# Kernel optimization log

Measured on AMD Instinct MI355X. Metric: run time of the kernel, lower is better.

The kernel has to match this reference:

```python
import jax, jax.numpy as jnp
import numpy as np

B, N, F = 4096, 128, 3
EPS = 1e-5


def _bn(x, g, b):
    # BatchNorm1d(element_num) on [B, N, C]: channels are dim 1 (the N elements);
    # training-mode stats over dims (0, 2), biased variance (torch default).
    m = x.mean(axis=(0, 2), keepdims=True)
    v = ((x - m) ** 2).mean(axis=(0, 2), keepdims=True)
    return (x - m) / jnp.sqrt(v + EPS) * g[None, :, None] + b[None, :, None]


def _rel(x, W, bvec, psi, phi, wr):
    # f'_i = wr/N * sum_{j != i} (psi*phi * <x_i, x_j>) * relu(unary(x_j))
    n = x.shape[1]
    U = jax.nn.relu(jnp.einsum('bnd,ed->bne', x, W) + bvec)       # [B,N,D]
    S = (psi * phi) * jnp.einsum('bnd,bmd->bnm', x, x)            # [B,N,N]
    S = S * (1.0 - jnp.eye(n, dtype=x.dtype))                     # exclude j == i
    return wr * jnp.einsum('bnm,bmd->bnd', S, U) / n


def setup_inputs() -> dict:
    key = jax.random.key(0)
    ks = iter(jax.random.split(key, 64))
    d1, d2 = 2 * F, 4 * F  # 6, 12

    def w(shape, s=0.1):
        return (jax.random.normal(next(ks), shape, dtype=jnp.float32) * s)

    def scalar():
        return jax.random.uniform(next(ks), (), dtype=jnp.float32)

    inp = {
        'x': jax.random.normal(next(ks), (B, N, F), dtype=jnp.float32),
        'fc1_w': w((d1, F)), 'fc1_b': w((d1,)),
        'bn1_g': jnp.ones((N,), jnp.float32), 'bn1_b': jnp.zeros((N,), jnp.float32),
        'fc2_w': w((d2, d1)), 'fc2_b': w((d2,)),
        'bn2_g': jnp.ones((N,), jnp.float32), 'bn2_b': jnp.zeros((N,), jnp.float32),
        'fc3_w': w((d2, d2)), 'fc3_b': w((d2,)),
        'u1_w': w((d2, d2)), 'u1_b': w((d2,)), 'ps1': scalar(), 'ph1': scalar(), 'wr1': scalar(),
        'u2_w': w((d2, d2)), 'u2_b': w((d2,)), 'ps2': scalar(), 'ph2': scalar(), 'wr2': scalar(),
        'u3_w': w((d2, d2)), 'u3_b': w((d2,)), 'ps3': scalar(), 'ph3': scalar(), 'wr3': scalar(),
        'u4_w': w((d2, d2)), 'u4_b': w((d2,)), 'ps4': scalar(), 'ph4': scalar(), 'wr4': scalar(),
        'fc4_w': w((d1, d2)), 'fc4_b': w((d1,)),
        'bn4_g': jnp.ones((N,), jnp.float32), 'bn4_b': jnp.zeros((N,), jnp.float32),
        'fc5_w': w((F, d1)), 'fc5_b': w((F,)),
        'fc6_w': w((1, F)), 'fc6_b': w((1,)),
        'fc7_w': w((F - 1, F)), 'fc7_b': w((F - 1,)),
        'fc8_w': w((1, F)), 'fc8_b': w((1,)),
    }
    return inp


def reference(x, fc1_w, fc1_b, bn1_g, bn1_b, fc2_w, fc2_b, bn2_g, bn2_b,
              fc3_w, fc3_b,
              u1_w, u1_b, ps1, ph1, wr1,
              u2_w, u2_b, ps2, ph2, wr2,
              u3_w, u3_b, ps3, ph3, wr3,
              u4_w, u4_b, ps4, ph4, wr4,
              fc4_w, fc4_b, bn4_g, bn4_b,
              fc5_w, fc5_b, fc6_w, fc6_b, fc7_w, fc7_b, fc8_w, fc8_b):
    h = jax.nn.relu(_bn(jnp.einsum('bnf,ef->bne', x, fc1_w) + fc1_b, bn1_g, bn1_b))
    h = jax.nn.relu(_bn(jnp.einsum('bnf,ef->bne', h, fc2_w) + fc2_b, bn2_g, bn2_b))
    h = jax.nn.sigmoid(jnp.einsum('bnf,ef->bne', h, fc3_w) + fc3_b)
    h = _rel(h, u1_w, u1_b, ps1, ph1, wr1)
    h = _rel(h, u2_w, u2_b, ps2, ph2, wr2)
    h = _rel(h, u3_w, u3_b, ps3, ph3, wr3)
    h = _rel(h, u4_w, u4_b, ps4, ph4, wr4)
    h = jax.nn.relu(_bn(jnp.einsum('bnf,ef->bne', h, fc4_w) + fc4_b, bn4_g, bn4_b))
    h = jax.nn.relu(jnp.einsum('bnf,ef->bne', h, fc5_w) + fc5_b)
    cls = jnp.einsum('bnf,ef->bne', h, fc6_w) + fc6_b          # [B,N,1]
    geo = jnp.einsum('bnf,ef->bne', h, fc7_w) + fc7_b          # [B,N,F-1]
    res = jnp.concatenate([cls, geo], axis=2)                   # [B,N,F]
    pres = res.max(axis=1)                                      # MaxPool1d over all N -> [B,F]
    pred = jax.nn.sigmoid(pres @ fc8_w.T + fc8_b)               # [B,1]
    return pred
```

## Files before the change

### kernel.cpp

```cpp
#include <hip/hip_runtime.h>
#include <hip/hip_fp16.h>

#define BB 4096
#define NN 128
#define EPS 1e-5f

#define ST_FLOATS 2560
#define A4_OFF ST_FLOATS

static __device__ __forceinline__ float sigmoidf_(float z){
  return 1.f/(1.f+__expf(-z));
}

__global__ __launch_bounds__(256) void k1(const float* __restrict__ x, const float* __restrict__ w1,
                   const float* __restrict__ b1, float* __restrict__ st){
  __shared__ float bl[512];
  const int t = threadIdx.x;
  const int tid = blockIdx.x*256 + t;
  const int n = tid & 127;
  float W[18], Bv[6];
  #pragma unroll
  for (int i=0;i<18;i++) W[i]=w1[i];
  #pragma unroll
  for (int i=0;i<6;i++) Bv[i]=b1[i];
  float s=0.f, sq=0.f;
  #pragma unroll
  for (int kk=0;kk<16;kk++){
    const int r = tid + kk*32768;
    const float* xr = x + (size_t)r*3;
    float x0=xr[0], x1=xr[1], x2=xr[2];
    #pragma unroll
    for (int e=0;e<6;e++){
      float a = fmaf(x0,W[e*3+0], fmaf(x1,W[e*3+1], fmaf(x2,W[e*3+2], Bv[e])));
      s+=a; sq=fmaf(a,a,sq);
    }
  }
  bl[t]=s; bl[256+t]=sq;
  __syncthreads();
  if (t<128){
    atomicAdd(&st[t], bl[t]+bl[t+128]);
  } else {
    const int tt=t-128;
    atomicAdd(&st[128+tt], bl[256+tt]+bl[256+tt+128]);
  }
}

__global__ __launch_bounds__(256) void k2(const float* __restrict__ x,
                   const float* __restrict__ w1, const float* __restrict__ b1,
                   const float* __restrict__ g1, const float* __restrict__ bb1,
                   const float* __restrict__ w2, const float* __restrict__ b2,
                   float* __restrict__ st){
  __shared__ float bl[512];
  const int t = threadIdx.x;
  const int tid = blockIdx.x*256 + t;
  const int n = tid & 127;
  const float mean = st[n]*(1.f/(BB*6));
  const float var  = st[128+n]*(1.f/(BB*6)) - mean*mean;
  const float sc = g1[n]*rsqrtf(var+EPS), sh = bb1[n]-mean*sc;
  float W1[18], B1v[6], W2[72], B2v[12];
  #pragma unroll
  for (int i=0;i<18;i++) W1[i]=w1[i];
  #pragma unroll
  for (int i=0;i<6;i++) B1v[i]=b1[i];
  #pragma unroll
  for (int i=0;i<72;i++) W2[i]=w2[i];
  #pragma unroll
  for (int i=0;i<12;i++) B2v[i]=b2[i];
  float s=0.f, sq=0.f;
  #pragma unroll
  for (int kk=0;kk<16;kk++){
    const int r = tid + kk*32768;
    const float* xr = x + (size_t)r*3;
    float x0=xr[0], x1=xr[1], x2=xr[2];
    float h[6];
    #pragma unroll
    for (int e=0;e<6;e++){
      float a = fmaf(x0,W1[e*3+0], fmaf(x1,W1[e*3+1], fmaf(x2,W1[e*3+2], B1v[e])));
      h[e]=fmaxf(fmaf(a,sc,sh),0.f);
    }
    #pragma unroll
    for (int d=0;d<12;d++){
      float z=B2v[d];
      #pragma unroll
      for (int e=0;e<6;e++) z=fmaf(h[e],W2[d*6+e],z);
      s+=z; sq=fmaf(z,z,sq);
    }
  }
  bl[t]=s; bl[256+t]=sq;
  __syncthreads();
  if (t<128){
    atomicAdd(&st[256+t], bl[t]+bl[t+128]);
  } else {
    const int tt=t-128;
    atomicAdd(&st[384+tt], bl[256+tt]+bl[256+tt+128]);
  }
}

__global__ __launch_bounds__(256,4) void k3(
  const float* __restrict__ x,
  const float* __restrict__ w1, const float* __restrict__ b1,
  const float* __restrict__ g1, const float* __restrict__ bb1,
  const float* __restrict__ w2, const float* __restrict__ b2,
  const float* __restrict__ g2, const float* __restrict__ bb2,
  const float* __restrict__ w3, const float* __restrict__ b3,
  const float* __restrict__ u1w, const float* __restrict__ u1b,
  const float* __restrict__ ps1, const float* __restrict__ ph1, const float* __restrict__ wr1,
  const float* __restrict__ u2w, const float* __restrict__ u2b,
  const float* __restrict__ ps2, const float* __restrict__ ph2, const float* __restrict__ wr2,
  const float* __restrict__ u3w, const float* __restrict__ u3b,
  const float* __restrict__ ps3, const float* __restrict__ ph3, const float* __restrict__ wr3,
  const float* __restrict__ u4w, const float* __restrict__ u4b,
  const float* __restrict__ ps4, const float* __restrict__ ph4, const float* __restrict__ wr4,
  const float* __restrict__ w4, const float* __restrict__ b4,
  float* __restrict__ a4, float* __restrict__ st)
{
  __shared__ float lds[4][2304];
  const int wave = threadIdx.x >> 6;
  const int lane = threadIdx.x & 63;
  const int b = blockIdx.x*4 + wave;
  float* Us = &lds[wave][0];
  __half* Xs = (__half*)&lds[wave][1536];
  const int r0 = lane*2, r1 = r0+1;

  const float inv1 = 1.f/(BB*6);
  const float m10 = st[r0]*inv1, v10 = st[128+r0]*inv1 - m10*m10;
  const float sA0 = g1[r0]*rsqrtf(v10+EPS), hA0 = bb1[r0]-m10*sA0;
  const float m11 = st[r1]*inv1, v11 = st[128+r1]*inv1 - m11*m11;
  const float sA1 = g1[r1]*rsqrtf(v11+EPS), hA1 = bb1[r1]-m11*sA1;
  const float inv2 = 1.f/(BB*12);
  const float m20 = st[256+r0]*inv2, v20 = st[384+r0]*inv2 - m20*m20;
  const float sB0 = g2[r0]*rsqrtf(v20+EPS), hB0 = bb2[r0]-m20*sB0;
  const float m21 = st[256+r1]*inv2, v21 = st[384+r1]*inv2 - m21*m21;
  const float sB1 = g2[r1]*rsqrtf(v21+EPS), hB1 = bb2[r1]-m21*sB1;

  const float2* xr = (const float2*)(x + ((size_t)b*128 + r0)*3);
  float2 q0v=xr[0], q1v=xr[1], q2v=xr[2], q3v=xr[3], q4v=xr[4], q5v=xr[5];
  const float xa0=q0v.x, xa1=q0v.y, xa2=q1v.x;
  const float xb0=q1v.y, xb1=q2v.x, xb2=q2v.y;
  (void)q3v; (void)q4v; (void)q5v;

  float h0[12], h1[12];
  {
    float g6a[6], g6b[6];
    #pragma unroll
    for (int e=0;e<6;e++){
      float a0 = fmaf(xa0,w1[e*3+0], fmaf(xa1,w1[e*3+1], fmaf(xa2,w1[e*3+2], b1[e])));
      float a1v= fmaf(xb0,w1[e*3+0], fmaf(xb1,w1[e*3+1], fmaf(xb2,w1[e*3+2], b1[e])));
      g6a[e]=fmaxf(fmaf(a0,sA0,hA0),0.f);
      g6b[e]=fmaxf(fmaf(a1v,sA1,hA1),0.f);
    }
    #pragma unroll
    for (int d=0;d<12;d++){
      float z0=b2[d], z1=b2[d];
      #pragma unroll
      for (int e=0;e<6;e++){ z0=fmaf(g6a[e],w2[d*6+e],z0); z1=fmaf(g6b[e],w2[d*6+e],z1); }
      h0[d]=fmaxf(fmaf(z0,sB0,hB0),0.f);
      h1[d]=fmaxf(fmaf(z1,sB1,hB1),0.f);
    }
  }

  float X0[12], X1[12];
  #pragma unroll
  for (int d=0; d<12; d++){
    float z0=b3[d], z1=b3[d];
    #pragma unroll
    for (int e=0;e<12;e++){ z0=fmaf(h0[e],w3[d*12+e],z0); z1=fmaf(h1[e],w3[d*12+e],z1); }
    X0[d]=sigmoidf_(z0); X1[d]=sigmoidf_(z1);
  }

  const float* UW[4]  = {u1w,u2w,u3w,u4w};
  const float* UBv[4] = {u1b,u2b,u3b,u4b};
  const float cf[4] = {
    wr1[0]*ps1[0]*ph1[0]*(1.f/128.f),
    wr2[0]*ps2[0]*ph2[0]*(1.f/128.f),
    wr3[0]*ps3[0]*ph3[0]*(1.f/128.f),
    wr4[0]*ps4[0]*ph4[0]*(1.f/128.f)
  };

  const int g = lane>>4;
  int kc = lane & 15; if (kc>11) kc=11;

  #pragma unroll
  for (int l=0;l<4;l++){
    const float* uw = UW[l];
    const float* ub = UBv[l];
    float U0[12], U1[12];
    #pragma unroll
    for (int d=0;d<12;d++){
      float z0=ub[d], z1=ub[d];
      #pragma unroll
      for (int e=0;e<12;e++){ z0=fmaf(X0[e],uw[d*12+e],z0); z1=fmaf(X1[e],uw[d*12+e],z1); }
      U0[d]=fmaxf(z0,0.f); U1[d]=fmaxf(z1,0.f);
    }
    float q0=0.f, q1=0.f;
    #pragma unroll
    for (int e=0;e<12;e++){ q0=fmaf(X0[e],X0[e],q0); q1=fmaf(X1[e],X1[e],q1); }

    float4* uwr = (float4*)(Us + r0*12);
    uwr[0]=make_float4(U0[0],U0[1],U0[2],U0[3]);
    uwr[1]=make_float4(U0[4],U0[5],U0[6],U0[7]);
    uwr[2]=make_float4(U0[8],U0[9],U0[10],U0[11]);
    uwr[3]=make_float4(U1[0],U1[1],U1[2],U1[3]);
    uwr[4]=make_float4(U1[4],U1[5],U1[6],U1[7]);
    uwr[5]=make_float4(U1[8],U1[9],U1[10],U1[11]);
    __half2 hp[12];
    #pragma unroll
    for (int i=0;i<6;i++) hp[i]   = __floats2half2_rn(X0[2*i],X0[2*i+1]);
    #pragma unroll
    for (int i=0;i<6;i++) hp[6+i] = __floats2half2_rn(X1[2*i],X1[2*i+1]);
    {
      const uint4* hpv = (const uint4*)hp;
      uint4* xw = (uint4*)(Xs + r0*12);
      xw[0]=hpv[0]; xw[1]=hpv[1]; xw[2]=hpv[2];
    }

    float mp[12];
    #pragma unroll
    for (int d=0;d<12;d++) mp[d]=0.f;
    #pragma unroll
    for (int i=0;i<32;i++){
      const int n = (g<<5) + ((i+g)&31);
      const float xv = __half2float(Xs[n*12 + kc]);
      const float4* up = (const float4*)(Us + n*12);
      float4 u0=up[0], u1=up[1], u2=up[2];
      mp[0]=fmaf(xv,u0.x,mp[0]); mp[1]=fmaf(xv,u0.y,mp[1]); mp[2]=fmaf(xv,u0.z,mp[2]); mp[3]=fmaf(xv,u0.w,mp[3]);
      mp[4]=fmaf(xv,u1.x,mp[4]); mp[5]=fmaf(xv,u1.y,mp[5]); mp[6]=fmaf(xv,u1.z,mp[6]); mp[7]=fmaf(xv,u1.w,mp[7]);
      mp[8]=fmaf(xv,u2.x,mp[8]); mp[9]=fmaf(xv,u2.y,mp[9]); mp[10]=fmaf(xv,u2.z,mp[10]); mp[11]=fmaf(xv,u2.w,mp[11]);
    }
    #pragma unroll
    for (int d=0;d<12;d++) mp[d] += __shfl_xor(mp[d], 16, 64);
    #pragma unroll
    for (int d=0;d<12;d++) mp[d] += __shfl_xor(mp[d], 32, 64);

    float Y0[12], Y1[12];
    #pragma unroll
    for (int d=0;d<12;d++){ Y0[d]=0.f; Y1[d]=0.f; }
    #pragma unroll
    for (int k=0;k<12;k++){
      const float xa = X0[k], xb = X1[k];
      #pragma unroll
      for (int d=0;d<12;d++){
        const float m = __int_as_float(__builtin_amdgcn_readlane(__float_as_int(mp[d]), k));
        Y0[d]=fmaf(xa,m,Y0[d]); Y1[d]=fmaf(xb,m,Y1[d]);
      }
    }
    const float coef = cf[l];
    #pragma unroll
    for (int d=0;d<12;d++){
      X0[d] = coef*(Y0[d] - q0*U0[d]);
      X1[d] = coef*(Y1[d] - q1*U1[d]);
    }
  }

  float z0[6], z1[6];
  float s0=0.f,sq0=0.f,s1=0.f,sq1=0.f;
  #pragma unroll
  for (int e=0;e<6;e++){
    float a0=b4[e], a1v=b4[e];
    #pragma unroll
    for (int d=0;d<12;d++){ a0=fmaf(X0[d],w4[e*12+d],a0); a1v=fmaf(X1[d],w4[e*12+d],a1v); }
    z0[e]=a0; z1[e]=a1v;
    s0+=a0; sq0=fmaf(a0,a0,sq0); s1+=a1v; sq1=fmaf(a1v,a1v,sq1);
  }
  float4* aw = (float4*)(a4 + ((size_t)b*128 + r0)*6);
  aw[0]=make_float4(z0[0],z0[1],z0[2],z0[3]);
  aw[1]=make_float4(z0[4],z0[5],z1[0],z1[1]);
  aw[2]=make_float4(z1[2],z1[3],z1[4],z1[5]);

  lds[wave][r0]=s0; lds[wave][r1]=s1;
  lds[wave][128+r0]=sq0; lds[wave][128+r1]=sq1;
  __syncthreads();
  const int t = threadIdx.x;
  const int c = (blockIdx.x & 7)*256;
  if (t < 128){
    float tot = lds[0][t]+lds[1][t]+lds[2][t]+lds[3][t];
    atomicAdd(&st[512 + c + t], tot);
  } else {
    const int tt = t-128;
    float tot = lds[0][128+tt]+lds[1][128+tt]+lds[2][128+tt]+lds[3][128+tt];
    atomicAdd(&st[512 + c + 128 + tt], tot);
  }
}

__global__ __launch_bounds__(256) void k4(
  const float* __restrict__ a4, const float* __restrict__ g4, const float* __restrict__ bb4,
  const float* __restrict__ w5, const float* __restrict__ b5,
  const float* __restrict__ w6, const float* __restrict__ b6,
  const float* __restrict__ w7, const float* __restrict__ b7,
  const float* __restrict__ w8, const float* __restrict__ b8,
  const float* __restrict__ st, float* __restrict__ out)
{
  const int wave = threadIdx.x>>6, lane = threadIdx.x&63;
  const int b = blockIdx.x*4 + wave;
  const int r0 = lane*2, r1 = r0+1;
  float ss0=0.f, qq0=0.f, ss1=0.f, qq1=0.f;
  #pragma unroll
  for (int cc=0;cc<8;cc++){
    ss0 += st[512+cc*256+r0];     qq0 += st[512+cc*256+128+r0];
    ss1 += st[512+cc*256+r1];     qq1 += st[512+cc*256+128+r1];
  }
  const float inv = 1.f/(BB*6);
  const float mean0 = ss0*inv, var0 = qq0*inv - mean0*mean0;
  const float sc0 = g4[r0]*rsqrtf(var0+EPS), sh0 = bb4[r0]-mean0*sc0;
  const float mean1 = ss1*inv, var1 = qq1*inv - mean1*mean1;
  const float sc1 = g4[r1]*rsqrtf(var1+EPS), sh1 = bb4[r1]-mean1*sc1;

  const float4* ar = (const float4*)(a4 + ((size_t)b*128 + r0)*6);
  float4 p0=ar[0], p1=ar[1], p2=ar[2];
  float h0[6] = {p0.x,p0.y,p0.z,p0.w,p1.x,p1.y};
  float h1[6] = {p1.z,p1.w,p2.x,p2.y,p2.z,p2.w};
  #pragma unroll
  for (int e=0;e<6;e++){
    h0[e]=fmaxf(fmaf(h0[e],sc0,sh0),0.f);
    h1[e]=fmaxf(fmaf(h1[e],sc1,sh1),0.f);
  }
  float m[3];
  {
    float h5a[3], h5b[3];
    #pragma unroll
    for (int f=0;f<3;f++){
      float za=b5[f], zb=b5[f];
      #pragma unroll
      for (int e=0;e<6;e++){ za=fmaf(h0[e],w5[f*6+e],za); zb=fmaf(h1[e],w5[f*6+e],zb); }
      h5a[f]=fmaxf(za,0.f); h5b[f]=fmaxf(zb,0.f);
    }
    float ca=b6[0], cb=b6[0];
    float g0a=b7[0], g0b=b7[0], g1a=b7[1], g1b=b7[1];
    #pragma unroll
    for (int f=0;f<3;f++){
      ca=fmaf(h5a[f],w6[f],ca);   cb=fmaf(h5b[f],w6[f],cb);
      g0a=fmaf(h5a[f],w7[f],g0a); g0b=fmaf(h5b[f],w7[f],g0b);
      g1a=fmaf(h5a[f],w7[3+f],g1a); g1b=fmaf(h5b[f],w7[3+f],g1b);
    }
    m[0]=fmaxf(ca,cb); m[1]=fmaxf(g0a,g0b); m[2]=fmaxf(g1a,g1b);
  }
  #pragma unroll
  for (int off=32; off>0; off>>=1){
    m[0]=fmaxf(m[0], __shfl_xor(m[0],off,64));
    m[1]=fmaxf(m[1], __shfl_xor(m[1],off,64));
    m[2]=fmaxf(m[2], __shfl_xor(m[2],off,64));
  }
  if (lane==0){
    float z = b8[0] + m[0]*w8[0] + m[1]*w8[1] + m[2]*w8[2];
    out[b]=sigmoidf_(z);
  }
}

extern "C" void kernel_launch(void* const* d_in, const int* in_sizes, int n_in,
                              void* d_out, int out_size, void* d_ws, size_t ws_size,
                              hipStream_t stream){
  const float* x   = (const float*)d_in[0];
  const float* f1w = (const float*)d_in[1];
  const float* f1b = (const float*)d_in[2];
  const float* g1  = (const float*)d_in[3];
  const float* bb1 = (const float*)d_in[4];
  const float* f2w = (const float*)d_in[5];
  const float* f2b = (const float*)d_in[6];
  const float* g2  = (const float*)d_in[7];
  const float* bb2 = (const float*)d_in[8];
  const float* f3w = (const float*)d_in[9];
  const float* f3b = (const float*)d_in[10];
  const float* u1w = (const float*)d_in[11];
  const float* u1b = (const float*)d_in[12];
  const float* ps1 = (const float*)d_in[13];
  const float* ph1 = (const float*)d_in[14];
  const float* wr1 = (const float*)d_in[15];
  const float* u2w = (const float*)d_in[16];
  const float* u2b = (const float*)d_in[17];
  const float* ps2 = (const float*)d_in[18];
  const float* ph2 = (const float*)d_in[19];
  const float* wr2 = (const float*)d_in[20];
  const float* u3w = (const float*)d_in[21];
  const float* u3b = (const float*)d_in[22];
  const float* ps3 = (const float*)d_in[23];
  const float* ph3 = (const float*)d_in[24];
  const float* wr3 = (const float*)d_in[25];
  const float* u4w = (const float*)d_in[26];
  const float* u4b = (const float*)d_in[27];
  const float* ps4 = (const float*)d_in[28];
  const float* ph4 = (const float*)d_in[29];
  const float* wr4 = (const float*)d_in[30];
  const float* f4w = (const float*)d_in[31];
  const float* f4b = (const float*)d_in[32];
  const float* g4  = (const float*)d_in[33];
  const float* bb4 = (const float*)d_in[34];
  const float* f5w = (const float*)d_in[35];
  const float* f5b = (const float*)d_in[36];
  const float* f6w = (const float*)d_in[37];
  const float* f6b = (const float*)d_in[38];
  const float* f7w = (const float*)d_in[39];
  const float* f7b = (const float*)d_in[40];
  const float* f8w = (const float*)d_in[41];
  const float* f8b = (const float*)d_in[42];

  float* wsf = (float*)d_ws;
  float* st  = wsf;
  float* a4  = wsf + A4_OFF;
  float* out = (float*)d_out;

  hipMemsetAsync(st, 0, ST_FLOATS*sizeof(float), stream);
  k1<<<dim3(128), dim3(256), 0, stream>>>(x, f1w, f1b, st);
  k2<<<dim3(128), dim3(256), 0, stream>>>(x, f1w, f1b, g1, bb1, f2w, f2b, st);
  k3<<<dim3(1024), dim3(256), 0, stream>>>(x, f1w, f1b, g1, bb1, f2w, f2b, g2, bb2,
      f3w, f3b,
      u1w,u1b,ps1,ph1,wr1, u2w,u2b,ps2,ph2,wr2,
      u3w,u3b,ps3,ph3,wr3, u4w,u4b,ps4,ph4,wr4,
      f4w, f4b, a4, st);
  k4<<<dim3(1024), dim3(256), 0, stream>>>(a4, g4, bb4, f5w, f5b,
      f6w, f6b, f7w, f7b, f8w, f8b, st, out);
}
```

Measured before the change: 220.4 us.

## Widen BN stat kernels to 1024 blocks with shadowed atomic accumulators

The BN1/BN2 statistics kernels now launch 1024 blocks with 2 rows per thread instead of 128 blocks looping 16 times, which spreads the work over more CUs. To limit contention on the atomics, each block adds into one of 8 shadow copies of the stat arrays, and consumers sum those copies. The main kernel drops its occupancy hint of 4 from launch bounds, scopes h0/h1 more tightly, and folds the -q*U term into the accumulator initialisation. It also adds a __syncthreads before reusing LDS for the partial stats. Consumers now do 8x more stat reads, and register allocation may shift without the occupancy hint.

```diff
diff --git a/kernel.cpp b/kernel.cpp
--- a/kernel.cpp
+++ b/kernel.cpp
@@ -5,8 +5,11 @@
 #define NN 128
 #define EPS 1e-5f
 
-#define ST_FLOATS 2560
-#define A4_OFF ST_FLOATS
+#define S1 0
+#define S2 2048
+#define S4 4096
+#define ST_FLOATS 6144
+#define A4_OFF 6144
 
 static __device__ __forceinline__ float sigmoidf_(float z){
   return 1.f/(1.f+__expf(-z));
@@ -17,7 +20,6 @@
   __shared__ float bl[512];
   const int t = threadIdx.x;
   const int tid = blockIdx.x*256 + t;
-  const int n = tid & 127;
   float W[18], Bv[6];
   #pragma unroll
   for (int i=0;i<18;i++) W[i]=w1[i];
@@ -25,8 +27,8 @@
   for (int i=0;i<6;i++) Bv[i]=b1[i];
   float s=0.f, sq=0.f;
   #pragma unroll
-  for (int kk=0;kk<16;kk++){
-    const int r = tid + kk*32768;
+  for (int kk=0;kk<2;kk++){
+    const int r = tid + kk*262144;
     const float* xr = x + (size_t)r*3;
     float x0=xr[0], x1=xr[1], x2=xr[2];
     #pragma unroll
@@ -37,12 +39,9 @@
   }
   bl[t]=s; bl[256+t]=sq;
   __syncthreads();
-  if (t<128){
-    atomicAdd(&st[t], bl[t]+bl[t+128]);
-  } else {
-    const int tt=t-128;
-    atomicAdd(&st[128+tt], bl[256+tt]+bl[256+tt+128]);
-  }
+  const int shadow = (blockIdx.x & 7)*256;
+  if (t<128) atomicAdd(&st[S1+shadow+t], bl[t]+bl[t+128]);
+  else       atomicAdd(&st[S1+shadow+t], bl[t+128]+bl[t+256]);
 }
 
 __global__ __launch_bounds__(256) void k2(const float* __restrict__ x,
@@ -53,9 +52,12 @@
   __shared__ float bl[512];
   const int t = threadIdx.x;
   const int tid = blockIdx.x*256 + t;
-  const int n = tid & 127;
-  const float mean = st[n]*(1.f/(BB*6));
-  const float var  = st[128+n]*(1.f/(BB*6)) - mean*mean;
+  const int n = t & 127;
+  float ss=0.f, qs=0.f;
+  #pragma unroll
+  for (int c=0;c<8;c++){ ss+=st[S1+c*256+n]; qs+=st[S1+c*256+128+n]; }
+  const float mean = ss*(1.f/(BB*6));
+  const float var  = qs*(1.f/(BB*6)) - mean*mean;
   const float sc = g1[n]*rsqrtf(var+EPS), sh = bb1[n]-mean*sc;
   float W1[18], B1v[6], W2[72], B2v[12];
   #pragma unroll
@@ -68,8 +70,8 @@
   for (int i=0;i<12;i++) B2v[i]=b2[i];
   float s=0.f, sq=0.f;
   #pragma unroll
-  for (int kk=0;kk<16;kk++){
-    const int r = tid + kk*32768;
+  for (int kk=0;kk<2;kk++){
+    const int r = tid + kk*262144;
     const float* xr = x + (size_t)r*3;
     float x0=xr[0], x1=xr[1], x2=xr[2];
     float h[6];
@@ -88,15 +90,12 @@
   }
   bl[t]=s; bl[256+t]=sq;
   __syncthreads();
-  if (t<128){
-    atomicAdd(&st[256+t], bl[t]+bl[t+128]);
-  } else {
-    const int tt=t-128;
-    atomicAdd(&st[384+tt], bl[256+tt]+bl[256+tt+128]);
-  }
-}
-
-__global__ __launch_bounds__(256,4) void k3(
+  const int shadow = (blockIdx.x & 7)*256;
+  if (t<128) atomicAdd(&st[S2+shadow+t], bl[t]+bl[t+128]);
+  else       atomicAdd(&st[S2+shadow+t], bl[t+128]+bl[t+256]);
+}
+
+__global__ __launch_bounds__(256) void k3(
   const float* __restrict__ x,
   const float* __restrict__ w1, const float* __restrict__ b1,
   const float* __restrict__ g1, const float* __restrict__ bb1,
@@ -122,24 +121,30 @@
   __half* Xs = (__half*)&lds[wave][1536];
   const int r0 = lane*2, r1 = r0+1;
 
-  const float inv1 = 1.f/(BB*6);
-  const float m10 = st[r0]*inv1, v10 = st[128+r0]*inv1 - m10*m10;
-  const float sA0 = g1[r0]*rsqrtf(v10+EPS), hA0 = bb1[r0]-m10*sA0;
-  const float m11 = st[r1]*inv1, v11 = st[128+r1]*inv1 - m11*m11;
-  const float sA1 = g1[r1]*rsqrtf(v11+EPS), hA1 = bb1[r1]-m11*sA1;
-  const float inv2 = 1.f/(BB*12);
-  const float m20 = st[256+r0]*inv2, v20 = st[384+r0]*inv2 - m20*m20;
-  const float sB0 = g2[r0]*rsqrtf(v20+EPS), hB0 = bb2[r0]-m20*sB0;
-  const float m21 = st[256+r1]*inv2, v21 = st[384+r1]*inv2 - m21*m21;
-  const float sB1 = g2[r1]*rsqrtf(v21+EPS), hB1 = bb2[r1]-m21*sB1;
+  float s1a=0,q1a=0,s1b=0,q1b=0,s2a=0,q2a=0,s2b=0,q2b=0;
+  #pragma unroll
+  for (int c=0;c<8;c++){
+    s1a+=st[S1+c*256+r0]; q1a+=st[S1+c*256+128+r0];
+    s1b+=st[S1+c*256+r1]; q1b+=st[S1+c*256+128+r1];
+    s2a+=st[S2+c*256+r0]; q2a+=st[S2+c*256+128+r0];
+    s2b+=st[S2+c*256+r1]; q2b+=st[S2+c*256+128+r1];
+  }
+  const float inv1 = 1.f/(BB*6), inv2 = 1.f/(BB*12);
+  float m = s1a*inv1, v = q1a*inv1 - m*m;
+  const float sA0 = g1[r0]*rsqrtf(v+EPS), hA0 = bb1[r0]-m*sA0;
+  m = s1b*inv1; v = q1b*inv1 - m*m;
+  const float sA1 = g1[r1]*rsqrtf(v+EPS), hA1 = bb1[r1]-m*sA1;
+  m = s2a*inv2; v = q2a*inv2 - m*m;
+  const float sB0 = g2[r0]*rsqrtf(v+EPS), hB0 = bb2[r0]-m*sB0;
+  m = s2b*inv2; v = q2b*inv2 - m*m;
+  const float sB1 = g2[r1]*rsqrtf(v+EPS), hB1 = bb2[r1]-m*sB1;
 
   const float2* xr = (const float2*)(x + ((size_t)b*128 + r0)*3);
-  float2 q0v=xr[0], q1v=xr[1], q2v=xr[2], q3v=xr[3], q4v=xr[4], q5v=xr[5];
-  const float xa0=q0v.x, xa1=q0v.y, xa2=q1v.x;
-  const float xb0=q1v.y, xb1=q2v.x, xb2=q2v.y;
-  (void)q3v; (void)q4v; (void)q5v;
-
-  float h0[12], h1[12];
+  float2 c0=xr[0], c1=xr[1], c2=xr[2];
+  const float xa0=c0.x, xa1=c0.y, xa2=c1.x;
+  const float xb0=c1.y, xb1=c2.x, xb2=c2.y;
+
+  float X0[12], X1[12];
   {
     float g6a[6], g6b[6];
     #pragma unroll
@@ -149,6 +154,7 @@
       g6a[e]=fmaxf(fmaf(a0,sA0,hA0),0.f);
       g6b[e]=fmaxf(fmaf(a1v,sA1,hA1),0.f);
     }
+    float h0[12], h1[12];
     #pragma unroll
     for (int d=0;d<12;d++){
       float z0=b2[d], z1=b2[d];
@@ -157,15 +163,13 @@
       h0[d]=fmaxf(fmaf(z0,sB0,hB0),0.f);
       h1[d]=fmaxf(fmaf(z1,sB1,hB1),0.f);
     }
-  }
-
-  float X0[12], X1[12];
-  #pragma unroll
-  for (int d=0; d<12; d++){
-    float z0=b3[d], z1=b3[d];
-    #pragma unroll
-    for (int e=0;e<12;e++){ z0=fmaf(h0[e],w3[d*12+e],z0); z1=fmaf(h1[e],w3[d*12+e],z1); }
-    X0[d]=sigmoidf_(z0); X1[d]=sigmoidf_(z1);
+    #pragma unroll
+    for (int d=0; d<12; d++){
+      float z0=b3[d], z1=b3[d];
+      #pragma unroll
+      for (int e=0;e<12;e++){ z0=fmaf(h0[e],w3[d*12+e],z0); z1=fmaf(h1[e],w3[d*12+e],z1); }
+      X0[d]=sigmoidf_(z0); X1[d]=sigmoidf_(z1);
+    }
   }
 
   const float* UW[4]  = {u1w,u2w,u3w,u4w};
@@ -184,34 +188,38 @@
   for (int l=0;l<4;l++){
     const float* uw = UW[l];
     const float* ub = UBv[l];
-    float U0[12], U1[12];
-    #pragma unroll
-    for (int d=0;d<12;d++){
-      float z0=ub[d], z1=ub[d];
-      #pragma unroll
-      for (int e=0;e<12;e++){ z0=fmaf(X0[e],uw[d*12+e],z0); z1=fmaf(X1[e],uw[d*12+e],z1); }
-      U0[d]=fmaxf(z0,0.f); U1[d]=fmaxf(z1,0.f);
-    }
-    float q0=0.f, q1=0.f;
-    #pragma unroll
-    for (int e=0;e<12;e++){ q0=fmaf(X0[e],X0[e],q0); q1=fmaf(X1[e],X1[e],q1); }
-
-    float4* uwr = (float4*)(Us + r0*12);
-    uwr[0]=make_float4(U0[0],U0[1],U0[2],U0[3]);
-    uwr[1]=make_float4(U0[4],U0[5],U0[6],U0[7]);
-    uwr[2]=make_float4(U0[8],U0[9],U0[10],U0[11]);
-    uwr[3]=make_float4(U1[0],U1[1],U1[2],U1[3]);
-    uwr[4]=make_float4(U1[4],U1[5],U1[6],U1[7]);
-    uwr[5]=make_float4(U1[8],U1[9],U1[10],U1[11]);
-    __half2 hp[12];
-    #pragma unroll
-    for (int i=0;i<6;i++) hp[i]   = __floats2half2_rn(X0[2*i],X0[2*i+1]);
-    #pragma unroll
-    for (int i=0;i<6;i++) hp[6+i] = __floats2half2_rn(X1[2*i],X1[2*i+1]);
+    float Y0[12], Y1[12];
     {
-      const uint4* hpv = (const uint4*)hp;
-      uint4* xw = (uint4*)(Xs + r0*12);
-      xw[0]=hpv[0]; xw[1]=hpv[1]; xw[2]=hpv[2];
+      float U0[12], U1[12];
+      #pragma unroll
+      for (int d=0;d<12;d++){
+        float z0=ub[d], z1=ub[d];
+        #pragma unroll
+        for (int e=0;e<12;e++){ z0=fmaf(X0[e],uw[d*12+e],z0); z1=fmaf(X1[e],uw[d*12+e],z1); }
+        U0[d]=fmaxf(z0,0.f); U1[d]=fmaxf(z1,0.f);
+      }
+      float q0=0.f, q1=0.f;
+      #pragma unroll
+      for (int e=0;e<12;e++){ q0=fmaf(X0[e],X0[e],q0); q1=fmaf(X1[e],X1[e],q1); }
+      float4* uwr = (float4*)(Us + r0*12);
+      uwr[0]=make_float4(U0[0],U0[1],U0[2],U0[3]);
+      uwr[1]=make_float4(U0[4],U0[5],U0[6],U0[7]);
+      uwr[2]=make_float4(U0[8],U0[9],U0[10],U0[11]);
+      uwr[3]=make_float4(U1[0],U1[1],U1[2],U1[3]);
+      uwr[4]=make_float4(U1[4],U1[5],U1[6],U1[7]);
+      uwr[5]=make_float4(U1[8],U1[9],U1[10],U1[11]);
+      __half2 hp[12];
+      #pragma unroll
+      for (int i=0;i<6;i++) hp[i]   = __floats2half2_rn(X0[2*i],X0[2*i+1]);
+      #pragma unroll
+      for (int i=0;i<6;i++) hp[6+i] = __floats2half2_rn(X1[2*i],X1[2*i+1]);
+      {
+        const uint4* hpv = (const uint4*)hp;
+        uint4* xw = (uint4*)(Xs + r0*12);
+        xw[0]=hpv[0]; xw[1]=hpv[1]; xw[2]=hpv[2];
+      }
+      #pragma unroll
+      for (int d=0;d<12;d++){ Y0[d] = -q0*U0[d]; Y1[d] = -q1*U1[d]; }
     }
 
     float mp[12];
@@ -232,24 +240,18 @@
     #pragma unroll
     for (int d=0;d<12;d++) mp[d] += __shfl_xor(mp[d], 32, 64);
 
-    float Y0[12], Y1[12];
-    #pragma unroll
-    for (int d=0;d<12;d++){ Y0[d]=0.f; Y1[d]=0.f; }
     #pragma unroll
     for (int k=0;k<12;k++){
       const float xa = X0[k], xb = X1[k];
       #pragma unroll
       for (int d=0;d<12;d++){
-        const float m = __int_as_float(__builtin_amdgcn_readlane(__float_as_int(mp[d]), k));
-        Y0[d]=fmaf(xa,m,Y0[d]); Y1[d]=fmaf(xb,m,Y1[d]);
+        const float mv = __int_as_float(__builtin_amdgcn_readlane(__float_as_int(mp[d]), k));
+        Y0[d]=fmaf(xa,mv,Y0[d]); Y1[d]=fmaf(xb,mv,Y1[d]);
       }
     }
     const float coef = cf[l];
     #pragma unroll
-    for (int d=0;d<12;d++){
-      X0[d] = coef*(Y0[d] - q0*U0[d]);
-      X1[d] = coef*(Y1[d] - q1*U1[d]);
-    }
+    for (int d=0;d<12;d++){ X0[d]=coef*Y0[d]; X1[d]=coef*Y1[d]; }
   }
 
   float z0[6], z1[6];
@@ -267,19 +269,13 @@
   aw[1]=make_float4(z0[4],z0[5],z1[0],z1[1]);
   aw[2]=make_float4(z1[2],z1[3],z1[4],z1[5]);
 
+  __syncthreads();
   lds[wave][r0]=s0; lds[wave][r1]=s1;
   lds[wave][128+r0]=sq0; lds[wave][128+r1]=sq1;
   __syncthreads();
   const int t = threadIdx.x;
   const int c = (blockIdx.x & 7)*256;
-  if (t < 128){
-    float tot = lds[0][t]+lds[1][t]+lds[2][t]+lds[3][t];
-    atomicAdd(&st[512 + c + t], tot);
-  } else {
-    const int tt = t-128;
-    float tot = lds[0][128+tt]+lds[1][128+tt]+lds[2][128+tt]+lds[3][128+tt];
-    atomicAdd(&st[512 + c + 128 + tt], tot);
-  }
+  atomicAdd(&st[S4 + c + t], lds[0][t]+lds[1][t]+lds[2][t]+lds[3][t]);
 }
 
 __global__ __launch_bounds__(256) void k4(
@@ -296,8 +292,8 @@
   float ss0=0.f, qq0=0.f, ss1=0.f, qq1=0.f;
   #pragma unroll
   for (int cc=0;cc<8;cc++){
-    ss0 += st[512+cc*256+r0];     qq0 += st[512+cc*256+128+r0];
-    ss1 += st[512+cc*256+r1];     qq1 += st[512+cc*256+128+r1];
+    ss0 += st[S4+cc*256+r0];     qq0 += st[S4+cc*256+128+r0];
+    ss1 += st[S4+cc*256+r1];     qq1 += st[S4+cc*256+128+r1];
   }
   const float inv = 1.f/(BB*6);
   const float mean0 = ss0*inv, var0 = qq0*inv - mean0*mean0;
@@ -314,7 +310,7 @@
     h0[e]=fmaxf(fmaf(h0[e],sc0,sh0),0.f);
     h1[e]=fmaxf(fmaf(h1[e],sc1,sh1),0.f);
   }
-  float m[3];
+  float mx[3];
   {
     float h5a[3], h5b[3];
     #pragma unroll
@@ -332,16 +328,16 @@
       g0a=fmaf(h5a[f],w7[f],g0a); g0b=fmaf(h5b[f],w7[f],g0b);
       g1a=fmaf(h5a[f],w7[3+f],g1a); g1b=fmaf(h5b[f],w7[3+f],g1b);
     }
-    m[0]=fmaxf(ca,cb); m[1]=fmaxf(g0a,g0b); m[2]=fmaxf(g1a,g1b);
+    mx[0]=fmaxf(ca,cb); mx[1]=fmaxf(g0a,g0b); mx[2]=fmaxf(g1a,g1b);
   }
   #pragma unroll
   for (int off=32; off>0; off>>=1){
-    m[0]=fmaxf(m[0], __shfl_xor(m[0],off,64));
-    m[1]=fmaxf(m[1], __shfl_xor(m[1],off,64));
-    m[2]=fmaxf(m[2], __shfl_xor(m[2],off,64));
+    mx[0]=fmaxf(mx[0], __shfl_xor(mx[0],off,64));
+    mx[1]=fmaxf(mx[1], __shfl_xor(mx[1],off,64));
+    mx[2]=fmaxf(mx[2], __shfl_xor(mx[2],off,64));
   }
   if (lane==0){
-    float z = b8[0] + m[0]*w8[0] + m[1]*w8[1] + m[2]*w8[2];
+    float z = b8[0] + mx[0]*w8[0] + mx[1]*w8[1] + mx[2]*w8[2];
     out[b]=sigmoidf_(z);
   }
 }
@@ -399,8 +395,8 @@
   float* out = (float*)d_out;
 
   hipMemsetAsync(st, 0, ST_FLOATS*sizeof(float), stream);
-  k1<<<dim3(128), dim3(256), 0, stream>>>(x, f1w, f1b, st);
-  k2<<<dim3(128), dim3(256), 0, stream>>>(x, f1w, f1b, g1, bb1, f2w, f2b, st);
+  k1<<<dim3(1024), dim3(256), 0, stream>>>(x, f1w, f1b, st);
+  k2<<<dim3(1024), dim3(256), 0, stream>>>(x, f1w, f1b, g1, bb1, f2w, f2b, st);
   k3<<<dim3(1024), dim3(256), 0, stream>>>(x, f1w, f1b, g1, bb1, f2w, f2b, g2, bb2,
       f3w, f3b,
       u1w,u1b,ps1,ph1,wr1, u2w,u2b,ps2,ph2,wr2,
```

Result: no change. 223.4 us (+1.4%).
